# Kernel tuning notes

Hardware: AMD Instinct MI355X
Metric: run time of the kernel (lower is better)

Reference implementation:

```python
import jax, jax.numpy as jnp
import numpy as np

E = 1024
H = 16
HD = E // H  # 64


def setup_inputs() -> dict:
    key = jax.random.key(0)
    ks = jax.random.split(key, 5)
    x = jax.random.normal(ks[0], (2, 2048, E), dtype=jnp.float32)
    s = 1.0 / np.sqrt(E)
    W_qkv = jax.random.uniform(ks[1], (E, 3 * E), jnp.float32, -s, s)
    b_qkv = jax.random.uniform(ks[2], (3 * E,), jnp.float32, -s, s)
    W_out = jax.random.uniform(ks[3], (E, E), jnp.float32, -s, s)
    b_out = jax.random.uniform(ks[4], (E,), jnp.float32, -s, s)
    return {"x": x, "W_qkv": W_qkv, "b_qkv": b_qkv, "W_out": W_out, "b_out": b_out}


def reference(x, W_qkv, b_qkv, W_out, b_out):
    B, N, _ = x.shape
    scale = HD ** (-0.5)
    qkv = x @ W_qkv + b_qkv                         # [B, N, 3E]
    qkv = qkv.reshape(B, N, H, 3 * HD)              # torch layout: per-head 3*hd chunk
    qkv = qkv.transpose(0, 2, 1, 3)                 # [B, H, N, 3*hd]
    q, k, v = jnp.split(qkv, 3, axis=-1)            # each [B, H, N, hd]
    attn = jnp.einsum('bhqd,bhkd->bhqk', q, k) * scale
    attn = jax.nn.softmax(attn, axis=-1)            # dropout is identity in eval
    out = jnp.einsum('bhqk,bhkd->bhqd', attn, v)    # [B, H, N, hd]
    out = out.transpose(0, 2, 1, 3).reshape(B, N, E)
    return out @ W_out + b_out
```

## Files before the change

kernel.cpp:

```cpp
#include <hip/hip_runtime.h>


#define SEQ 2048
#define NH  16

typedef __attribute__((ext_vector_type(8))) short short8;
typedef __attribute__((ext_vector_type(4))) short short4v;
typedef __attribute__((ext_vector_type(4))) float floatx4;
typedef __attribute__((ext_vector_type(4))) _Float16 half4;
typedef __attribute__((ext_vector_type(8))) _Float16 half8;
typedef __attribute__((ext_vector_type(2))) _Float16 half2v;
typedef __attribute__((ext_vector_type(2))) __fp16 fp16x2;

#define QSCALE 0.1803368801111204f

__device__ __forceinline__ short f2bf(float f) {
    union { float f; unsigned u; } v; v.f = f;
    unsigned r = v.u + 0x7fffu + ((v.u >> 16) & 1u);
    return (short)(r >> 16);
}

__device__ __forceinline__ float fast_exp2(float x) {
#if __has_builtin(__builtin_amdgcn_exp2f)
    return __builtin_amdgcn_exp2f(x);
#else
    return exp2f(x);
#endif
}

__device__ __forceinline__ half2v cvt_pk(float a, float b) {
#if __has_builtin(__builtin_amdgcn_cvt_pkrtz)
    union { fp16x2 i; half2v o; } u;
    u.i = __builtin_amdgcn_cvt_pkrtz(a, b);
    return u.o;
#else
    half2v r; r.x = (_Float16)a; r.y = (_Float16)b; return r;
#endif
}

#define GLDS16(gp, lp)                                                          \
    __builtin_amdgcn_global_load_lds(                                           \
        (const __attribute__((address_space(1))) unsigned int*)(gp),            \
        (__attribute__((address_space(3))) unsigned int*)(lp), 16, 0, 0)

__global__ __launch_bounds__(256) void prep_kernel(
    const float* __restrict__ x,  short* __restrict__ xb,
    const float* __restrict__ wq, short* __restrict__ wqkvt,
    const float* __restrict__ wo, short* __restrict__ woutt)
{
    const int tid = threadIdx.x;
    const int b = blockIdx.x;
    if (b < 2048) {
        int i = b * 256 + tid;
        const float4* in4 = (const float4*)x + (size_t)i * 2;
        float4 a = in4[0], c = in4[1];
        short8 o = { f2bf(a.x), f2bf(a.y), f2bf(a.z), f2bf(a.w),
                     f2bf(c.x), f2bf(c.y), f2bf(c.z), f2bf(c.w) };
        *((short8*)xb + i) = o;
        return;
    }
    __shared__ float T[64][65];
    const float* in; short* out; int R, C, c0, r0;
    if (b < 2816) {
        int t = b - 2048; in = wq; out = wqkvt; R = 1024; C = 3072;
        c0 = (t % 48) * 64; r0 = (t / 48) * 64;
    } else {
        int t = b - 2816; in = wo; out = woutt; R = 1024; C = 1024;
        c0 = (t & 15) * 64; r0 = (t >> 4) * 64;
    }
#pragma unroll
    for (int it = 0; it < 4; ++it) {
        int r = it * 16 + (tid >> 4), c = (tid & 15) * 4;
        float4 v = *(const float4*)(in + (size_t)(r0 + r) * C + c0 + c);
        T[c+0][r] = v.x; T[c+1][r] = v.y; T[c+2][r] = v.z; T[c+3][r] = v.w;
    }
    __syncthreads();
#pragma unroll
    for (int it = 0; it < 4; ++it) {
        int oc = it * 16 + (tid >> 4), k = (tid & 15) * 4;
        short4v o = { f2bf(T[oc][k]), f2bf(T[oc][k+1]), f2bf(T[oc][k+2]), f2bf(T[oc][k+3]) };
        *(short4v*)(out + (size_t)(c0 + oc) * R + r0 + k) = o;
    }
}

__global__ __launch_bounds__(256) void vtrans_kernel(
    const _Float16* __restrict__ vn, _Float16* __restrict__ vfb)
{
    __shared__ _Float16 T[64][72];
    const int tid = threadIdx.x;
    const int bh = blockIdx.y, n0 = blockIdx.x * 64;
#pragma unroll
    for (int it = 0; it < 2; ++it) {
        int n = it * 32 + (tid >> 3), c = (tid & 7) * 8;
        const _Float16* p = vn + ((size_t)bh * SEQ + n0 + n) * 64 + c;
        half4 a = *(const half4*)(p);
        half4 b = *(const half4*)(p + 4);
        T[c+0][n] = a.x; T[c+1][n] = a.y; T[c+2][n] = a.z; T[c+3][n] = a.w;
        T[c+4][n] = b.x; T[c+5][n] = b.y; T[c+6][n] = b.z; T[c+7][n] = b.w;
    }
    __syncthreads();
#pragma unroll
    for (int it = 0; it < 2; ++it) {
        int idx = it * 256 + tid;
        int quad = idx & 3, d = (idx >> 2) & 63, u = idx >> 8;
        int dt = d >> 4, l16 = d & 15;
        const _Float16* row = &T[d][u * 32 + quad * 4];
        half4 lo = *(const half4*)(row);
        half4 hi = *(const half4*)(row + 16);
        _Float16* q = vfb + ((size_t)bh * 131072)
                          + (size_t)((n0 >> 5) + u) * 2048
                          + dt * 512 + l16 * 32 + quad * 8;
        *(half4*)(q)     = lo;
        *(half4*)(q + 4) = hi;
    }
}

#define GEMM_CORE(A_PTR, B_PTR, LDA, LDB)                                        \
    __shared__ short As[128 * 32];                                               \
    __shared__ short Bs[128 * 32];                                               \
    const int tid  = threadIdx.x;                                                \
    const int lane = tid & 63, w = tid >> 6;                                     \
    const int quad = lane >> 4, l16 = lane & 15;                                 \
    const int wm = w >> 1, wn = w & 1;                                           \
    const int c0 = blockIdx.x * 128, r0 = blockIdx.y * 128;                      \
    floatx4 acc[4][4];                                                           \
    _Pragma("unroll")                                                            \
    for (int i = 0; i < 4; ++i)                                                  \
        _Pragma("unroll")                                                        \
        for (int j = 0; j < 4; ++j) acc[i][j] = (floatx4){0.f, 0.f, 0.f, 0.f};   \
    const int srow = tid >> 2;                                                   \
    const int sgx  = ((tid & 3) ^ ((srow >> 1) & 3)) * 8;                        \
    const short* Ag = (A_PTR) + (size_t)(r0 + srow) * (LDA) + sgx;               \
    const short* Bg = (B_PTR) + (size_t)(c0 + srow) * (LDB) + sgx;               \
    const int fsw = (l16 >> 1) & 3;                                              \
    for (int kk = 0; kk < 1024; kk += 32) {                                      \
        __syncthreads();                                                         \
        GLDS16(Ag + kk,                      As + tid * 8);                      \
        GLDS16(Ag + (size_t)64 * (LDA) + kk, As + 2048 + tid * 8);               \
        GLDS16(Bg + kk,                      Bs + tid * 8);                      \
        GLDS16(Bg + (size_t)64 * (LDB) + kk, Bs + 2048 + tid * 8);               \
        __syncthreads();                                                         \
        short8 af[4], bf[4];                                                     \
        _Pragma("unroll")                                                        \
        for (int mt = 0; mt < 4; ++mt)                                           \
            af[mt] = *(const short8*)&As[(wm * 64 + mt * 16 + l16) * 32 + (quad ^ fsw) * 8]; \
        _Pragma("unroll")                                                        \
        for (int nt = 0; nt < 4; ++nt)                                           \
            bf[nt] = *(const short8*)&Bs[(wn * 64 + nt * 16 + l16) * 32 + (quad ^ fsw) * 8]; \
        _Pragma("unroll")                                                        \
        for (int mt = 0; mt < 4; ++mt)                                           \
            _Pragma("unroll")                                                    \
            for (int nt = 0; nt < 4; ++nt)                                       \
                acc[mt][nt] = __builtin_amdgcn_mfma_f32_16x16x32_bf16(           \
                    af[mt], bf[nt], acc[mt][nt], 0, 0, 0);                       \
    }

__global__ __launch_bounds__(256) void qkv_gemm_kernel(
    const short* __restrict__ wt, const short* __restrict__ xb,
    const float* __restrict__ bias,
    short* __restrict__ qb, short* __restrict__ kb, _Float16* __restrict__ vnb)
{
    GEMM_CORE(wt, xb, 1024, 1024)
#pragma unroll
    for (int mt = 0; mt < 4; ++mt) {
        int oc0 = r0 + wm * 64 + mt * 16 + quad * 4;
        int head = oc0 / 192;
        int t = (oc0 - head * 192) >> 6;
        int d0 = oc0 & 63;
        float4 bv = *(const float4*)(bias + oc0);
#pragma unroll
        for (int nt = 0; nt < 4; ++nt) {
            int tok = c0 + wn * 64 + nt * 16 + l16;
            int bh = (tok >> 11) * NH + head;
            size_t base = ((size_t)bh * SEQ + (tok & (SEQ - 1))) * 64 + d0;
            float v0 = acc[mt][nt][0] + bv.x, v1 = acc[mt][nt][1] + bv.y;
            float v2 = acc[mt][nt][2] + bv.z, v3 = acc[mt][nt][3] + bv.w;
            if (t == 0) {
                short4v o = { f2bf(v0 * QSCALE), f2bf(v1 * QSCALE),
                              f2bf(v2 * QSCALE), f2bf(v3 * QSCALE) };
                *(short4v*)(qb + base) = o;
            } else if (t == 1) {
                short4v o = { f2bf(v0), f2bf(v1), f2bf(v2), f2bf(v3) };
                *(short4v*)(kb + base) = o;
            } else {
                half4 o = { (_Float16)v0, (_Float16)v1, (_Float16)v2, (_Float16)v3 };
                *(half4*)(vnb + base) = o;
            }
        }
    }
}

__global__ __launch_bounds__(512) void out_gemm_kernel(
    const short* __restrict__ wt, const short* __restrict__ ab,
    const float* __restrict__ bias, float* __restrict__ out)
{
    __shared__ short As[128 * 32];
    __shared__ short Bs[128 * 32];
    const int tid  = threadIdx.x;
    const int lane = tid & 63, w = tid >> 6;
    const int quad = lane >> 4, l16 = lane & 15;
    const int wm = w >> 2, wn = w & 3;
    const int c0 = blockIdx.x * 128, r0 = blockIdx.y * 128;
    floatx4 acc[4][2];
#pragma unroll
    for (int i = 0; i < 4; ++i)
#pragma unroll
        for (int j = 0; j < 2; ++j) acc[i][j] = (floatx4){0.f, 0.f, 0.f, 0.f};
    const int srow = tid >> 2;
    const int sgx  = ((tid & 3) ^ ((srow >> 1) & 3)) * 8;
    const short* Ag = wt + (size_t)(r0 + srow) * 1024 + sgx;
    const short* Bg = ab + (size_t)(c0 + srow) * 1024 + sgx;
    const int fsw = (l16 >> 1) & 3;
    for (int kk = 0; kk < 1024; kk += 32) {
        __syncthreads();
        GLDS16(Ag + kk, As + tid * 8);
        GLDS16(Bg + kk, Bs + tid * 8);
        __syncthreads();
        short8 af[4], bf[2];
#pragma unroll
        for (int mt = 0; mt < 4; ++mt)
            af[mt] = *(const short8*)&As[(wm * 64 + mt * 16 + l16) * 32 + (quad ^ fsw) * 8];
#pragma unroll
        for (int nt = 0; nt < 2; ++nt)
            bf[nt] = *(const short8*)&Bs[(wn * 32 + nt * 16 + l16) * 32 + (quad ^ fsw) * 8];
#pragma unroll
        for (int mt = 0; mt < 4; ++mt)
#pragma unroll
            for (int nt = 0; nt < 2; ++nt)
                acc[mt][nt] = __builtin_amdgcn_mfma_f32_16x16x32_bf16(
                    af[mt], bf[nt], acc[mt][nt], 0, 0, 0);
    }
#pragma unroll
    for (int mt = 0; mt < 4; ++mt) {
        int oc0 = r0 + wm * 64 + mt * 16 + quad * 4;
        float4 bv = *(const float4*)(bias + oc0);
#pragma unroll
        for (int nt = 0; nt < 2; ++nt) {
            int tok = c0 + wn * 32 + nt * 16 + l16;
            float4 o = { acc[mt][nt][0] + bv.x, acc[mt][nt][1] + bv.y,
                         acc[mt][nt][2] + bv.z, acc[mt][nt][3] + bv.w };
            *(float4*)(out + (size_t)tok * 1024 + oc0) = o;
        }
    }
}

__global__ __launch_bounds__(256, 4) void attn_kernel(
    const short* __restrict__ qb, const short* __restrict__ kb,
    const _Float16* __restrict__ vfb, short* __restrict__ ob)
{
    __shared__ short Ks[128 * 64];
    __shared__ float Ls[4][32];
    const int tid  = threadIdx.x;
    const int lane = tid & 63, w = tid >> 6;
    const int quad = lane >> 4, l16 = lane & 15;
    const int qh = w >> 1, kq = w & 1;
    const int lb = blockIdx.x;
    const int bh = (lb & 7) + (((lb >> 3) & 3) << 3);
    const int q0 = (lb >> 5) * 64;

    short8 aq[2][2];
#pragma unroll
    for (int qf = 0; qf < 2; ++qf) {
        const short* qp = qb + ((size_t)bh * SEQ + q0 + qh * 32 + qf * 16 + l16) * 64 + quad * 8;
        aq[qf][0] = *(const short8*)(qp);
        aq[qf][1] = *(const short8*)(qp + 32);
    }

    const int krow = tid >> 3, kg = tid & 7;
    const short* kgp = kb + ((size_t)bh * SEQ + krow) * 64 + (kg ^ (krow & 7)) * 8;
    const _Float16* vfp = vfb + (size_t)bh * 131072 + l16 * 32 + quad * 8;

    floatx4 o_acc[4][2];
#pragma unroll
    for (int dt = 0; dt < 4; ++dt)
#pragma unroll
        for (int qf = 0; qf < 2; ++qf) o_acc[dt][qf] = (floatx4){0.f, 0.f, 0.f, 0.f};
    float lw[2] = {0.f, 0.f};

    for (int k0 = 0; k0 < SEQ; k0 += 128) {
        __syncthreads();
        const short* kc_p = kgp + (size_t)k0 * 64;
        GLDS16(kc_p,        Ks + tid * 8);
        GLDS16(kc_p + 2048, Ks + 2048 + tid * 8);
        GLDS16(kc_p + 4096, Ks + 4096 + tid * 8);
        GLDS16(kc_p + 6144, Ks + 6144 + tid * 8);
        __syncthreads();

#pragma unroll
        for (int uu = 0; uu < 2; ++uu) {
            const int u = kq * 2 + uu;
            const _Float16* vu = vfp + (size_t)((k0 >> 5) + u) * 2048;
            half8 av8[4];
#pragma unroll
            for (int dt = 0; dt < 4; ++dt) {
                union { short8 s; half8 h; } vv;
                vv.s = *(const short8*)(vu + dt * 512);
                av8[dt] = vv.h;
            }
            floatx4 sacc[2][2];
#pragma unroll
            for (int h = 0; h < 2; ++h) {
                const short* krp = &Ks[(u * 32 + h * 16 + l16) * 64];
                short8 ak0 = *(const short8*)(krp + ((0 + quad) ^ (l16 & 7)) * 8);
                short8 ak1 = *(const short8*)(krp + ((4 + quad) ^ (l16 & 7)) * 8);
                __builtin_amdgcn_s_setprio(1);
#pragma unroll
                for (int qf = 0; qf < 2; ++qf) {
                    floatx4 z = (floatx4){0.f, 0.f, 0.f, 0.f};
                    z = __builtin_amdgcn_mfma_f32_16x16x32_bf16(ak0, aq[qf][0], z, 0, 0, 0);
                    sacc[h][qf] = __builtin_amdgcn_mfma_f32_16x16x32_bf16(ak1, aq[qf][1], z, 0, 0, 0);
                }
                __builtin_amdgcn_s_setprio(0);
            }
            half8 pf8[2];
#pragma unroll
            for (int qf = 0; qf < 2; ++qf) {
                float p0 = fast_exp2(sacc[0][qf][0]);
                float p1 = fast_exp2(sacc[0][qf][1]);
                float p2 = fast_exp2(sacc[0][qf][2]);
                float p3 = fast_exp2(sacc[0][qf][3]);
                float p4 = fast_exp2(sacc[1][qf][0]);
                float p5 = fast_exp2(sacc[1][qf][1]);
                float p6 = fast_exp2(sacc[1][qf][2]);
                float p7 = fast_exp2(sacc[1][qf][3]);
                lw[qf] += ((p0 + p1) + (p2 + p3)) + ((p4 + p5) + (p6 + p7));
                half2v a = cvt_pk(p0, p1), b = cvt_pk(p2, p3);
                half2v c = cvt_pk(p4, p5), d = cvt_pk(p6, p7);
                pf8[qf] = (half8){a.x, a.y, b.x, b.y, c.x, c.y, d.x, d.y};
            }
            __builtin_amdgcn_s_setprio(1);
#pragma unroll
            for (int dt = 0; dt < 4; ++dt)
#pragma unroll
                for (int qf = 0; qf < 2; ++qf)
                    o_acc[dt][qf] = __builtin_amdgcn_mfma_f32_16x16x32_f16(
                        av8[dt], pf8[qf], o_acc[dt][qf], 0, 0, 0);
            __builtin_amdgcn_s_setprio(0);
        }
    }

#pragma unroll
    for (int qf = 0; qf < 2; ++qf) {
        lw[qf] += __shfl_xor(lw[qf], 16);
        lw[qf] += __shfl_xor(lw[qf], 32);
        if (quad == 0) Ls[w][qf * 16 + l16] = lw[qf];
    }

    float* Red = (float*)Ks;
    __syncthreads();
#pragma unroll
    for (int dt = 0; dt < 4; ++dt)
#pragma unroll
        for (int qf = 0; qf < 2; ++qf) {
            int fi = (((qh * 2 + qf) * 4 + dt) * 64 + lane) * 4;
            if (kq == 1) *(floatx4*)&Red[fi] = o_acc[dt][qf];
        }
    __syncthreads();
    if (kq == 0) {
        float inv[2];
#pragma unroll
        for (int qf = 0; qf < 2; ++qf) {
            int qi = qf * 16 + l16;
            inv[qf] = 1.0f / (Ls[qh * 2 + 0][qi] + Ls[qh * 2 + 1][qi]);
        }
        const int b = bh >> 4, h = bh & 15;
#pragma unroll
        for (int dt = 0; dt < 4; ++dt)
#pragma unroll
            for (int qf = 0; qf < 2; ++qf) {
                int fi = (((qh * 2 + qf) * 4 + dt) * 64 + lane) * 4;
                floatx4 o = o_acc[dt][qf] + *(const floatx4*)&Red[fi];
                int tok = b * SEQ + q0 + qh * 32 + qf * 16 + l16;
                short4v o4 = { f2bf(o[0] * inv[qf]), f2bf(o[1] * inv[qf]),
                               f2bf(o[2] * inv[qf]), f2bf(o[3] * inv[qf]) };
                *(short4v*)(ob + (size_t)tok * 1024 + h * 64 + dt * 16 + quad * 4) = o4;
            }
    }
}

extern "C" void kernel_launch(void* const* d_in, const int* in_sizes, int n_in,
                              void* d_out, int out_size, void* d_ws, size_t ws_size,
                              hipStream_t stream) {
    const float* x     = (const float*)d_in[0];
    const float* W_qkv = (const float*)d_in[1];
    const float* b_qkv = (const float*)d_in[2];
    const float* W_out = (const float*)d_in[3];
    const float* b_out = (const float*)d_in[4];
    float* out = (float*)d_out;

    short* xb      = (short*)d_ws;
    short* wqkvt   = xb    + (size_t)4096 * 1024;
    short* woutt   = wqkvt + (size_t)3072 * 1024;
    short* qb      = woutt + (size_t)1024 * 1024;
    short* kb      = qb    + (size_t)32 * SEQ * 64;
    _Float16* vnb  = (_Float16*)(kb + (size_t)32 * SEQ * 64);
    _Float16* vfb  = vnb + (size_t)32 * SEQ * 64;
    short* ob      = (short*)(vfb + (size_t)32 * 64 * SEQ);

    prep_kernel<<<3072, 256, 0, stream>>>(x, xb, W_qkv, wqkvt, W_out, woutt);
    qkv_gemm_kernel<<<dim3(32, 24), 256, 0, stream>>>(wqkvt, xb, b_qkv, qb, kb, vnb);
    vtrans_kernel<<<dim3(32, 32), 256, 0, stream>>>(vnb, vfb);
    attn_kernel<<<1024, 256, 0, stream>>>(qb, kb, vfb, ob);
    out_gemm_kernel<<<dim3(32, 8), 512, 0, stream>>>(woutt, ob, b_out, out);
}
```

Baseline: 185.9 us.

## Fuse V transpose into QKV GEMM epilogue and stage V tiles in LDS

Removes the separate vtrans kernel: the QKV GEMM epilogue now writes V straight into the swizzled, MFMA-ready layout the attention kernel needs, using scattered 2-byte stores. The attention kernel now loads each 128-key V tile into shared memory with async global-to-LDS copies alongside K, and reads fragments from LDS with an XOR swizzle instead of from global memory. This saves one kernel launch and a full round trip of V through memory. In exchange it adds uncoalesced scalar stores in the GEMM epilogue and 16KB more LDS per attention block, which may lower occupancy.

New measurement: 182.1 us. -2.0%, faster.

```diff
diff --git a/kernel.cpp b/kernel.cpp
--- a/kernel.cpp
+++ b/kernel.cpp
@@ -80,38 +80,6 @@
         int oc = it * 16 + (tid >> 4), k = (tid & 15) * 4;
         short4v o = { f2bf(T[oc][k]), f2bf(T[oc][k+1]), f2bf(T[oc][k+2]), f2bf(T[oc][k+3]) };
         *(short4v*)(out + (size_t)(c0 + oc) * R + r0 + k) = o;
-    }
-}
-
-__global__ __launch_bounds__(256) void vtrans_kernel(
-    const _Float16* __restrict__ vn, _Float16* __restrict__ vfb)
-{
-    __shared__ _Float16 T[64][72];
-    const int tid = threadIdx.x;
-    const int bh = blockIdx.y, n0 = blockIdx.x * 64;
-#pragma unroll
-    for (int it = 0; it < 2; ++it) {
-        int n = it * 32 + (tid >> 3), c = (tid & 7) * 8;
-        const _Float16* p = vn + ((size_t)bh * SEQ + n0 + n) * 64 + c;
-        half4 a = *(const half4*)(p);
-        half4 b = *(const half4*)(p + 4);
-        T[c+0][n] = a.x; T[c+1][n] = a.y; T[c+2][n] = a.z; T[c+3][n] = a.w;
-        T[c+4][n] = b.x; T[c+5][n] = b.y; T[c+6][n] = b.z; T[c+7][n] = b.w;
-    }
-    __syncthreads();
-#pragma unroll
-    for (int it = 0; it < 2; ++it) {
-        int idx = it * 256 + tid;
-        int quad = idx & 3, d = (idx >> 2) & 63, u = idx >> 8;
-        int dt = d >> 4, l16 = d & 15;
-        const _Float16* row = &T[d][u * 32 + quad * 4];
-        half4 lo = *(const half4*)(row);
-        half4 hi = *(const half4*)(row + 16);
-        _Float16* q = vfb + ((size_t)bh * 131072)
-                          + (size_t)((n0 >> 5) + u) * 2048
-                          + dt * 512 + l16 * 32 + quad * 8;
-        *(half4*)(q)     = lo;
-        *(half4*)(q + 4) = hi;
     }
 }
 
@@ -158,7 +126,7 @@
 __global__ __launch_bounds__(256) void qkv_gemm_kernel(
     const short* __restrict__ wt, const short* __restrict__ xb,
     const float* __restrict__ bias,
-    short* __restrict__ qb, short* __restrict__ kb, _Float16* __restrict__ vnb)
+    short* __restrict__ qb, short* __restrict__ kb, _Float16* __restrict__ vfb)
 {
     GEMM_CORE(wt, xb, 1024, 1024)
 #pragma unroll
@@ -172,19 +140,32 @@
         for (int nt = 0; nt < 4; ++nt) {
             int tok = c0 + wn * 64 + nt * 16 + l16;
             int bh = (tok >> 11) * NH + head;
-            size_t base = ((size_t)bh * SEQ + (tok & (SEQ - 1))) * 64 + d0;
             float v0 = acc[mt][nt][0] + bv.x, v1 = acc[mt][nt][1] + bv.y;
             float v2 = acc[mt][nt][2] + bv.z, v3 = acc[mt][nt][3] + bv.w;
-            if (t == 0) {
-                short4v o = { f2bf(v0 * QSCALE), f2bf(v1 * QSCALE),
-                              f2bf(v2 * QSCALE), f2bf(v3 * QSCALE) };
-                *(short4v*)(qb + base) = o;
-            } else if (t == 1) {
-                short4v o = { f2bf(v0), f2bf(v1), f2bf(v2), f2bf(v3) };
-                *(short4v*)(kb + base) = o;
+            if (t == 2) {
+                int n  = tok & (SEQ - 1);
+                int h  = nt & 1;
+                int qv = l16 >> 2, r = l16 & 3;
+                int j  = h * 4 + r;
+                size_t vb = (size_t)bh * 131072 + (size_t)(n >> 7) * 8192
+                          + (size_t)((n >> 5) & 3) * 2048 + (size_t)d0 * 32 + j;
+                _Float16 vv[4] = { (_Float16)v0, (_Float16)v1,
+                                   (_Float16)v2, (_Float16)v3 };
+#pragma unroll
+                for (int jj = 0; jj < 4; ++jj) {
+                    int cset = qv ^ (((d0 + jj) >> 1) & 3);
+                    vfb[vb + jj * 32 + cset * 8] = vv[jj];
+                }
             } else {
-                half4 o = { (_Float16)v0, (_Float16)v1, (_Float16)v2, (_Float16)v3 };
-                *(half4*)(vnb + base) = o;
+                size_t base = ((size_t)bh * SEQ + (tok & (SEQ - 1))) * 64 + d0;
+                if (t == 0) {
+                    short4v o = { f2bf(v0 * QSCALE), f2bf(v1 * QSCALE),
+                                  f2bf(v2 * QSCALE), f2bf(v3 * QSCALE) };
+                    *(short4v*)(qb + base) = o;
+                } else {
+                    short4v o = { f2bf(v0), f2bf(v1), f2bf(v2), f2bf(v3) };
+                    *(short4v*)(kb + base) = o;
+                }
             }
         }
     }
@@ -248,8 +229,9 @@
     const short* __restrict__ qb, const short* __restrict__ kb,
     const _Float16* __restrict__ vfb, short* __restrict__ ob)
 {
-    __shared__ short Ks[128 * 64];
-    __shared__ float Ls[4][32];
+    __shared__ short    Ks[128 * 64];
+    __shared__ _Float16 Vts[64 * 128];
+    __shared__ float    Ls[4][32];
     const int tid  = threadIdx.x;
     const int lane = tid & 63, w = tid >> 6;
     const int quad = lane >> 4, l16 = lane & 15;
@@ -268,7 +250,7 @@
 
     const int krow = tid >> 3, kg = tid & 7;
     const short* kgp = kb + ((size_t)bh * SEQ + krow) * 64 + (kg ^ (krow & 7)) * 8;
-    const _Float16* vfp = vfb + (size_t)bh * 131072 + l16 * 32 + quad * 8;
+    const short* vgp = (const short*)(vfb + (size_t)bh * 131072) + tid * 8;
 
     floatx4 o_acc[4][2];
 #pragma unroll
@@ -284,17 +266,22 @@
         GLDS16(kc_p + 2048, Ks + 2048 + tid * 8);
         GLDS16(kc_p + 4096, Ks + 4096 + tid * 8);
         GLDS16(kc_p + 6144, Ks + 6144 + tid * 8);
+        const short* vc_p = vgp + (size_t)k0 * 64;
+        GLDS16(vc_p,        (short*)Vts + tid * 8);
+        GLDS16(vc_p + 2048, (short*)Vts + 2048 + tid * 8);
+        GLDS16(vc_p + 4096, (short*)Vts + 4096 + tid * 8);
+        GLDS16(vc_p + 6144, (short*)Vts + 6144 + tid * 8);
         __syncthreads();
 
 #pragma unroll
         for (int uu = 0; uu < 2; ++uu) {
             const int u = kq * 2 + uu;
-            const _Float16* vu = vfp + (size_t)((k0 >> 5) + u) * 2048;
             half8 av8[4];
 #pragma unroll
             for (int dt = 0; dt < 4; ++dt) {
                 union { short8 s; half8 h; } vv;
-                vv.s = *(const short8*)(vu + dt * 512);
+                vv.s = *(const short8*)((const short*)Vts + u * 2048
+                        + (dt * 16 + l16) * 32 + (quad ^ ((l16 >> 1) & 3)) * 8);
                 av8[dt] = vv.h;
             }
             floatx4 sacc[2][2];
@@ -393,13 +380,11 @@
     short* woutt   = wqkvt + (size_t)3072 * 1024;
     short* qb      = woutt + (size_t)1024 * 1024;
     short* kb      = qb    + (size_t)32 * SEQ * 64;
-    _Float16* vnb  = (_Float16*)(kb + (size_t)32 * SEQ * 64);
-    _Float16* vfb  = vnb + (size_t)32 * SEQ * 64;
+    _Float16* vfb  = (_Float16*)(kb + (size_t)32 * SEQ * 64);
     short* ob      = (short*)(vfb + (size_t)32 * 64 * SEQ);
 
     prep_kernel<<<3072, 256, 0, stream>>>(x, xb, W_qkv, wqkvt, W_out, woutt);
-    qkv_gemm_kernel<<<dim3(32, 24), 256, 0, stream>>>(wqkvt, xb, b_qkv, qb, kb, vnb);
-    vtrans_kernel<<<dim3(32, 32), 256, 0, stream>>>(vnb, vfb);
+    qkv_gemm_kernel<<<dim3(32, 24), 256, 0, stream>>>(wqkvt, xb, b_qkv, qb, kb, vfb);
     attn_kernel<<<1024, 256, 0, stream>>>(qb, kb, vfb, ob);
     out_gemm_kernel<<<dim3(32, 8), 512, 0, stream>>>(woutt, ob, b_out, out);
 }
```
